# Performance work log

Measured on AMD Instinct MI355X. Metric: run time of the kernel, lower is better.

Reference implementation:

```python
import jax, jax.numpy as jnp
import numpy as np

N = 40000
IN_DIM = 128
HID = 64
E = 640000


def sage_conv(x, edge_index, W_l, b_l, W_r):
    """PyG SAGEConv with mean aggregation.
    out = lin_l(mean_{j in N(i)} x_j) + lin_r(x_i)
    edge_index[0]=src (message source), edge_index[1]=dst (aggregation target).
    """
    src, dst = edge_index[0], edge_index[1]
    n = x.shape[0]
    msgs = x[src]                                            # [E, d] gather
    sums = jax.ops.segment_sum(msgs, dst, num_segments=n)    # [N, d]
    cnt = jax.ops.segment_sum(jnp.ones((msgs.shape[0],), x.dtype), dst,
                              num_segments=n)                # [N]
    mean = sums / jnp.maximum(cnt, 1.0)[:, None]
    return mean @ W_l.T + b_l + x @ W_r.T


def setup_inputs() -> dict:
    key = jax.random.key(0)
    ks = jax.random.split(key, 8)
    x = jax.random.normal(ks[0], (N, IN_DIM), dtype=jnp.float32)
    edge_index = jax.random.randint(ks[1], (2, E), 0, N, dtype=jnp.int32)
    s1 = 1.0 / np.sqrt(IN_DIM)
    s2 = 1.0 / np.sqrt(HID)
    W1_l = jax.random.uniform(ks[2], (HID, IN_DIM), jnp.float32, -s1, s1)
    b1_l = jax.random.uniform(ks[3], (HID,), jnp.float32, -s1, s1)
    W1_r = jax.random.uniform(ks[4], (HID, IN_DIM), jnp.float32, -s1, s1)
    W2_l = jax.random.uniform(ks[5], (HID, HID), jnp.float32, -s2, s2)
    b2_l = jax.random.uniform(ks[6], (HID,), jnp.float32, -s2, s2)
    W2_r = jax.random.uniform(ks[7], (HID, HID), jnp.float32, -s2, s2)
    return {"x": x, "edge_index": edge_index,
            "W1_l": W1_l, "b1_l": b1_l, "W1_r": W1_r,
            "W2_l": W2_l, "b2_l": b2_l, "W2_r": W2_r}


def reference(x, edge_index, W1_l, b1_l, W1_r, W2_l, b2_l, W2_r):
    h = sage_conv(x, edge_index, W1_l, b1_l, W1_r)
    h = jax.nn.relu(h)
    # dropout is identity in eval mode (reference baseline is deterministic)
    z = sage_conv(h, edge_index, W2_l, b2_l, W2_r)
    return z
```

## Files before the change

kernel.cpp:

```cpp
#include <hip/hip_runtime.h>

#define INDIM 128
#define HID 64
#define CAP 64
#define GEMM_BLOCKS 625
#define BIN_BLOCKS 256
#define PREP_BLOCKS 32
#define RSH 7
#define RMASK ((1 << RSH) - 1)
#define NRANGE 313
#define SBCAP 28

__device__ __forceinline__ float bf2f(unsigned short u) {
    union { unsigned int i; float f; } c; c.i = ((unsigned int)u) << 16; return c.f;
}
__device__ __forceinline__ unsigned short f2bf(float f) {
    union { float f; unsigned int i; } c; c.f = f;
    return (unsigned short)((c.i + 0x7FFFu + ((c.i >> 16) & 1u)) >> 16);
}

__device__ __forceinline__ float4 gather4(const unsigned short* __restrict__ Pb,
                                          int row, int f4) {
    const uint2 v = *(const uint2*)&Pb[(size_t)row * 64 + f4 * 4];
    float4 r;
    r.x = bf2f((unsigned short)(v.x & 0xffffu));
    r.y = bf2f((unsigned short)(v.x >> 16));
    r.z = bf2f((unsigned short)(v.y & 0xffffu));
    r.w = bf2f((unsigned short)(v.y >> 16));
    return r;
}

__device__ __forceinline__ float4 agg_core(const unsigned short* __restrict__ Pb,
                                           int idx0, int deg, int q, int f4) {
    float4 acc = make_float4(0.f, 0.f, 0.f, 0.f);
    const int nchunk = (deg + 3) >> 2;
    for (int c = 0; c < nchunk; c += 4) {
        #pragma unroll
        for (int u = 0; u < 4; ++u) {
            const int cc = c + u;
            const int lanesel = cc * 4 + q;
            const int sidx = __shfl(idx0, lanesel, 64);
            const float m = (cc < nchunk && lanesel < deg) ? 1.f : 0.f;
            const float4 v = gather4(Pb, sidx, f4);
            acc.x += v.x * m; acc.y += v.y * m;
            acc.z += v.z * m; acc.w += v.w * m;
        }
    }
    acc.x += __shfl_xor(acc.x, 16, 64); acc.y += __shfl_xor(acc.y, 16, 64);
    acc.z += __shfl_xor(acc.z, 16, 64); acc.w += __shfl_xor(acc.w, 16, 64);
    acc.x += __shfl_xor(acc.x, 32, 64); acc.y += __shfl_xor(acc.y, 32, 64);
    acc.z += __shfl_xor(acc.z, 32, 64); acc.w += __shfl_xor(acc.w, 32, 64);
    return acc;
}


__global__ __launch_bounds__(256) void k_bin_prep(
    const int* __restrict__ src, const int* __restrict__ dst,
    unsigned int* __restrict__ hist_global, unsigned int* __restrict__ ebin,
    const float* __restrict__ W1l, const float* __restrict__ W1r,
    const float* __restrict__ W2l, const float* __restrict__ W2r,
    float* __restrict__ WT1l, float* __restrict__ WT1r,
    float* __restrict__ WT2l, float* __restrict__ WT2r, int E) {
    const int tid = threadIdx.x;

    if (blockIdx.x >= BIN_BLOCKS) {
        const int gtid = (blockIdx.x - BIN_BLOCKS) * 256 + tid;
        if (gtid < 64 * 128) {
            int j = gtid >> 7, k = gtid & 127;
            WT1l[k * 64 + j] = W1l[gtid];
            WT1r[k * 64 + j] = W1r[gtid];
        }
        if (gtid < 64 * 64) {
            int j = gtid >> 6, k = gtid & 63;
            WT2l[k * 64 + j] = W2l[gtid];
            WT2r[k * 64 + j] = W2r[gtid];
        }
        return;
    }

    __shared__ unsigned int hist[NRANGE];
    __shared__ unsigned int cur[NRANGE];
    const int b = blockIdx.x;
    const int ech = (E + BIN_BLOCKS - 1) / BIN_BLOCKS;
    const int e0 = b * ech;
    const int e1 = (e0 + ech < E) ? e0 + ech : E;

    for (int r = tid; r < NRANGE; r += 256) { hist[r] = 0; cur[r] = 0; }
    __syncthreads();
    for (int e = e0 + tid; e < e1; e += 256)
        atomicAdd(&hist[((unsigned)dst[e]) >> RSH], 1u);
    __syncthreads();
    for (int r = tid; r < NRANGE; r += 256)
        hist_global[(size_t)r * BIN_BLOCKS + b] = hist[r];
    __syncthreads();
    for (int e = e0 + tid; e < e1; e += 256) {
        const unsigned d = (unsigned)dst[e];
        const unsigned s = (unsigned)src[e];
        const unsigned r = d >> RSH;
        const unsigned off = atomicAdd(&cur[r], 1u);
        if (off < SBCAP)
            ebin[((size_t)r * BIN_BLOCKS + b) * SBCAP + off] = (d << 16) | s;
    }
}


__global__ __launch_bounds__(256) void k_gemm1_place(
    const float* __restrict__ A,
    const float* __restrict__ WTl, const float* __restrict__ WTr,
    unsigned short* __restrict__ Pb, float* __restrict__ Q,
    const unsigned int* __restrict__ hist_global,
    const unsigned int* __restrict__ ebin,
    int* __restrict__ cnt, unsigned short* __restrict__ sorted, int N) {
    __shared__ float As[64][INDIM + 1];
    __shared__ unsigned int lcnt[1 << RSH];
    const int tid = threadIdx.x;

    if (blockIdx.x >= GEMM_BLOCKS) {
        const int r = blockIdx.x - GEMM_BLOCKS;
        if (tid < (1 << RSH)) lcnt[tid] = 0;
        __syncthreads();
        unsigned c = hist_global[(size_t)r * BIN_BLOCKS + tid];
        if (c > SBCAP) c = SBCAP;
        const unsigned int* eb = ebin + ((size_t)r * BIN_BLOCKS + tid) * SBCAP;
        for (unsigned i = 0; i < c; ++i) {
            const unsigned p = eb[i];
            const unsigned d = p >> 16;
            const unsigned slot = atomicAdd(&lcnt[d & RMASK], 1u);
            if (slot < CAP)
                sorted[(d << 6) + slot] = (unsigned short)(p & 0xffffu);
        }
        __syncthreads();
        for (int l = tid; l < (1 << RSH); l += 256) {
            const int node = (r << RSH) + l;
            if (node < N) cnt[node] = (int)lcnt[l];
        }
        return;
    }

    const int bm = blockIdx.x * 64;
    for (int idx = tid; idx < 64 * 32; idx += 256) {
        int row = idx >> 5, kq = idx & 31;
        const float4 v = ((const float4*)A)[(size_t)(bm + row) * 32 + kq];
        As[row][kq * 4 + 0] = v.x; As[row][kq * 4 + 1] = v.y;
        As[row][kq * 4 + 2] = v.z; As[row][kq * 4 + 3] = v.w;
    }
    __syncthreads();

    const int tx = tid & 15, ty = tid >> 4;
    const int n0 = ty * 4;
    float accl[4][4] = {}, accr[4][4] = {};
    #pragma unroll 8
    for (int k = 0; k < INDIM; ++k) {
        float a[4];
        #pragma unroll
        for (int i = 0; i < 4; ++i) a[i] = As[n0 + i][k];
        const float4 blv = ((const float4*)WTl)[k * 16 + tx];
        const float4 brv = ((const float4*)WTr)[k * 16 + tx];
        const float bl[4] = {blv.x, blv.y, blv.z, blv.w};
        const float br[4] = {brv.x, brv.y, brv.z, brv.w};
        #pragma unroll
        for (int i = 0; i < 4; ++i) {
            #pragma unroll
            for (int j = 0; j < 4; ++j) {
                accl[i][j] += a[i] * bl[j];
                accr[i][j] += a[i] * br[j];
            }
        }
    }
    #pragma unroll
    for (int i = 0; i < 4; ++i) {
        int m = bm + n0 + i;
        ushort4 pv;
        pv.x = f2bf(accl[i][0]); pv.y = f2bf(accl[i][1]);
        pv.z = f2bf(accl[i][2]); pv.w = f2bf(accl[i][3]);
        ((ushort4*)Pb)[(size_t)m * 16 + tx] = pv;
        ((float4*)Q)[(size_t)m * 16 + tx] =
            make_float4(accr[i][0], accr[i][1], accr[i][2], accr[i][3]);
    }
}


__global__ __launch_bounds__(256) void k_agg1(
    const unsigned short* __restrict__ Pb, const float* __restrict__ Q,
    const float* __restrict__ b1,
    const int* __restrict__ cnt, const unsigned short* __restrict__ sorted,
    float* __restrict__ H, int N) {
    const int wid  = (blockIdx.x * 256 + threadIdx.x) >> 6;
    const int lane = threadIdx.x & 63;
    const int q = lane >> 4, f4 = lane & 15;
    if (wid >= N) return;
    int deg = cnt[wid]; if (deg > CAP) deg = CAP;
    const int ls = (lane < deg) ? lane : ((deg > 0) ? deg - 1 : 0);
    const int idx0 = (deg > 0) ? (int)sorted[(wid << 6) + ls] : 0;
    const float4 a = agg_core(Pb, idx0, deg, q, f4);
    if (q == 0) {
        const float inv = 1.0f / fmaxf((float)deg, 1.0f);
        const float4 qv = *(const float4*)&Q[(size_t)wid * 64 + f4 * 4];
        const float4 bv = *(const float4*)&b1[f4 * 4];
        float4 hv;
        hv.x = fmaxf(a.x * inv + bv.x + qv.x, 0.f);
        hv.y = fmaxf(a.y * inv + bv.y + qv.y, 0.f);
        hv.z = fmaxf(a.z * inv + bv.z + qv.z, 0.f);
        hv.w = fmaxf(a.w * inv + bv.w + qv.w, 0.f);
        *(float4*)&H[(size_t)wid * 64 + f4 * 4] = hv;
    }
}


__global__ __launch_bounds__(256) void k_gemm2(
    const float* __restrict__ H,
    const float* __restrict__ WTl, const float* __restrict__ WTr,
    unsigned short* __restrict__ Pb2, float* __restrict__ Q2, int N) {
    __shared__ float As[64][HID + 1];
    const int tid = threadIdx.x;
    const int bm = blockIdx.x * 64;
    for (int idx = tid; idx < 64 * 16; idx += 256) {
        int row = idx >> 4, kq = idx & 15;
        const float4 v = ((const float4*)H)[(size_t)(bm + row) * 16 + kq];
        As[row][kq * 4 + 0] = v.x; As[row][kq * 4 + 1] = v.y;
        As[row][kq * 4 + 2] = v.z; As[row][kq * 4 + 3] = v.w;
    }
    __syncthreads();

    const int tx = tid & 15, ty = tid >> 4;
    const int n0 = ty * 4;
    float accl[4][4] = {}, accr[4][4] = {};
    #pragma unroll 8
    for (int k = 0; k < HID; ++k) {
        float a[4];
        #pragma unroll
        for (int i = 0; i < 4; ++i) a[i] = As[n0 + i][k];
        const float4 blv = ((const float4*)WTl)[k * 16 + tx];
        const float4 brv = ((const float4*)WTr)[k * 16 + tx];
        const float bl[4] = {blv.x, blv.y, blv.z, blv.w};
        const float br[4] = {brv.x, brv.y, brv.z, brv.w};
        #pragma unroll
        for (int i = 0; i < 4; ++i) {
            #pragma unroll
            for (int j = 0; j < 4; ++j) {
                accl[i][j] += a[i] * bl[j];
                accr[i][j] += a[i] * br[j];
            }
        }
    }
    #pragma unroll
    for (int i = 0; i < 4; ++i) {
        int m = bm + n0 + i;
        if (m < N) {
            ushort4 pv;
            pv.x = f2bf(accl[i][0]); pv.y = f2bf(accl[i][1]);
            pv.z = f2bf(accl[i][2]); pv.w = f2bf(accl[i][3]);
            ((ushort4*)Pb2)[(size_t)m * 16 + tx] = pv;
            ((float4*)Q2)[(size_t)m * 16 + tx] =
                make_float4(accr[i][0], accr[i][1], accr[i][2], accr[i][3]);
        }
    }
}


__global__ __launch_bounds__(256) void k_agg2(
    const unsigned short* __restrict__ Pb2, const float* __restrict__ Q2,
    const float* __restrict__ b2,
    const int* __restrict__ cnt, const unsigned short* __restrict__ sorted,
    float* __restrict__ z, int N) {
    const int wid  = (blockIdx.x * 256 + threadIdx.x) >> 6;
    const int lane = threadIdx.x & 63;
    const int q = lane >> 4, f4 = lane & 15;
    if (wid >= N) return;
    int deg = cnt[wid]; if (deg > CAP) deg = CAP;
    const int ls = (lane < deg) ? lane : ((deg > 0) ? deg - 1 : 0);
    const int idx0 = (deg > 0) ? (int)sorted[(wid << 6) + ls] : 0;
    const float4 a = agg_core(Pb2, idx0, deg, q, f4);
    if (q == 0) {
        const float inv = 1.0f / fmaxf((float)deg, 1.0f);
        const float4 qv = *(const float4*)&Q2[(size_t)wid * 64 + f4 * 4];
        const float4 bv = *(const float4*)&b2[f4 * 4];
        float4 zv;
        zv.x = a.x * inv + bv.x + qv.x;
        zv.y = a.y * inv + bv.y + qv.y;
        zv.z = a.z * inv + bv.z + qv.z;
        zv.w = a.w * inv + bv.w + qv.w;
        *(float4*)&z[(size_t)wid * 64 + f4 * 4] = zv;
    }
}


extern "C" void kernel_launch(void* const* d_in, const int* in_sizes, int n_in,
                              void* d_out, int out_size, void* d_ws, size_t ws_size,
                              hipStream_t stream) {
    const float* x   = (const float*)d_in[0];
    const int*  edge = (const int*)d_in[1];
    const float* W1l = (const float*)d_in[2];
    const float* b1l = (const float*)d_in[3];
    const float* W1r = (const float*)d_in[4];
    const float* W2l = (const float*)d_in[5];
    const float* b2l = (const float*)d_in[6];
    const float* W2r = (const float*)d_in[7];

    const int N = in_sizes[0] / INDIM;
    const int E = in_sizes[1] / 2;
    const int* src = edge;
    const int* dst = edge + E;

    char* w = (char*)d_ws;
    auto carve = [&](size_t bytes) {
        char* p = w; w += (bytes + 255) & ~(size_t)255; return p;
    };
    unsigned short* Pb  = (unsigned short*)carve((size_t)N * 64 * 2);
    float* Q    = (float*)carve((size_t)N * 64 * 4);
    float* WT1l = (float*)carve(128 * 64 * 4);
    float* WT1r = (float*)carve(128 * 64 * 4);
    float* WT2l = (float*)carve(64 * 64 * 4);
    float* WT2r = (float*)carve(64 * 64 * 4);
    int* cnt    = (int*)carve((size_t)N * 4);
    unsigned short* sorted = (unsigned short*)carve((size_t)N * CAP * 2);
    unsigned int* hist_global = (unsigned int*)carve((size_t)NRANGE * BIN_BLOCKS * 4);
    size_t ebin_bytes = (size_t)NRANGE * BIN_BLOCKS * SBCAP * 4;
    size_t H_bytes    = (size_t)N * 64 * 4;
    char* uni = carve(ebin_bytes > H_bytes ? ebin_bytes : H_bytes);
    unsigned int* ebin = (unsigned int*)uni;
    float* H           = (float*)uni;

    float* zout = (float*)d_out;

    const int gT = (N + 63) / 64;
    const int gW = (N * 64 + 255) / 256;

    k_bin_prep<<<BIN_BLOCKS + PREP_BLOCKS, 256, 0, stream>>>(
        src, dst, hist_global, ebin,
        W1l, W1r, W2l, W2r, WT1l, WT1r, WT2l, WT2r, E);
    k_gemm1_place<<<GEMM_BLOCKS + NRANGE, 256, 0, stream>>>(
        x, WT1l, WT1r, Pb, Q, hist_global, ebin, cnt, sorted, N);
    k_agg1<<<gW, 256, 0, stream>>>(Pb, Q, b1l, cnt, sorted, H, N);
    k_gemm2<<<gT, 256, 0, stream>>>(H, WT2l, WT2r, Pb, Q, N);
    k_agg2<<<gW, 256, 0, stream>>>(Pb, Q, b2l, cnt, sorted, zout, N);
}
```

Before: 118.5 us.

## Fuse layer-1 aggregation with layer-2 GEMM and widen gather to 16-byte loads

The layer-1 mean aggregation and the layer-2 GEMM now run in one 512-thread kernel: each block aggregates 64 nodes into shared memory and multiplies them directly, so the H intermediate never goes to global memory. Separate Pb2/Q2 buffers are added so the fused kernel can read Pb/Q while writing the layer-2 outputs without a race. The gather now loads 8 bf16 values (16 bytes) per lane, with 8 neighbours per step instead of 4. Block order in gemm1_place is swapped so the placement blocks are scheduled first. The costs are more workspace, fewer blocks in the fused kernel, and a serial loop over 8 nodes per wave that may cut latency hiding.

```diff
diff --git a/kernel.cpp b/kernel.cpp
--- a/kernel.cpp
+++ b/kernel.cpp
@@ -19,38 +19,34 @@
     return (unsigned short)((c.i + 0x7FFFu + ((c.i >> 16) & 1u)) >> 16);
 }
 
-__device__ __forceinline__ float4 gather4(const unsigned short* __restrict__ Pb,
-                                          int row, int f4) {
-    const uint2 v = *(const uint2*)&Pb[(size_t)row * 64 + f4 * 4];
-    float4 r;
-    r.x = bf2f((unsigned short)(v.x & 0xffffu));
-    r.y = bf2f((unsigned short)(v.x >> 16));
-    r.z = bf2f((unsigned short)(v.y & 0xffffu));
-    r.w = bf2f((unsigned short)(v.y >> 16));
-    return r;
-}
-
-__device__ __forceinline__ float4 agg_core(const unsigned short* __restrict__ Pb,
-                                           int idx0, int deg, int q, int f4) {
-    float4 acc = make_float4(0.f, 0.f, 0.f, 0.f);
-    const int nchunk = (deg + 3) >> 2;
-    for (int c = 0; c < nchunk; c += 4) {
-        #pragma unroll
-        for (int u = 0; u < 4; ++u) {
-            const int cc = c + u;
-            const int lanesel = cc * 4 + q;
+__device__ __forceinline__ void agg8(const unsigned short* __restrict__ Pb,
+                                     int idx0, int deg, int q, int f8,
+                                     float acc[8]) {
+    const int nstep = (deg + 7) >> 3;
+    for (int s = 0; s < nstep; s += 2) {
+        #pragma unroll
+        for (int u = 0; u < 2; ++u) {
+            const int ss = s + u;
+            const int lanesel = ss * 8 + q;
             const int sidx = __shfl(idx0, lanesel, 64);
-            const float m = (cc < nchunk && lanesel < deg) ? 1.f : 0.f;
-            const float4 v = gather4(Pb, sidx, f4);
-            acc.x += v.x * m; acc.y += v.y * m;
-            acc.z += v.z * m; acc.w += v.w * m;
-        }
-    }
-    acc.x += __shfl_xor(acc.x, 16, 64); acc.y += __shfl_xor(acc.y, 16, 64);
-    acc.z += __shfl_xor(acc.z, 16, 64); acc.w += __shfl_xor(acc.w, 16, 64);
-    acc.x += __shfl_xor(acc.x, 32, 64); acc.y += __shfl_xor(acc.y, 32, 64);
-    acc.z += __shfl_xor(acc.z, 32, 64); acc.w += __shfl_xor(acc.w, 32, 64);
-    return acc;
+            const float m = (ss < nstep && lanesel < deg) ? 1.f : 0.f;
+            const uint4 v = *(const uint4*)&Pb[(size_t)sidx * 64 + f8 * 8];
+            acc[0] += bf2f((unsigned short)(v.x & 0xffffu)) * m;
+            acc[1] += bf2f((unsigned short)(v.x >> 16)) * m;
+            acc[2] += bf2f((unsigned short)(v.y & 0xffffu)) * m;
+            acc[3] += bf2f((unsigned short)(v.y >> 16)) * m;
+            acc[4] += bf2f((unsigned short)(v.z & 0xffffu)) * m;
+            acc[5] += bf2f((unsigned short)(v.z >> 16)) * m;
+            acc[6] += bf2f((unsigned short)(v.w & 0xffffu)) * m;
+            acc[7] += bf2f((unsigned short)(v.w >> 16)) * m;
+        }
+    }
+    #pragma unroll
+    for (int j = 0; j < 8; ++j) {
+        acc[j] += __shfl_xor(acc[j], 8, 64);
+        acc[j] += __shfl_xor(acc[j], 16, 64);
+        acc[j] += __shfl_xor(acc[j], 32, 64);
+    }
 }
 
 
@@ -115,8 +111,8 @@
     __shared__ unsigned int lcnt[1 << RSH];
     const int tid = threadIdx.x;
 
-    if (blockIdx.x >= GEMM_BLOCKS) {
-        const int r = blockIdx.x - GEMM_BLOCKS;
+    if (blockIdx.x < NRANGE) {
+        const int r = blockIdx.x;
         if (tid < (1 << RSH)) lcnt[tid] = 0;
         __syncthreads();
         unsigned c = hist_global[(size_t)r * BIN_BLOCKS + tid];
@@ -137,7 +133,7 @@
         return;
     }
 
-    const int bm = blockIdx.x * 64;
+    const int bm = (blockIdx.x - NRANGE) * 64;
     for (int idx = tid; idx < 64 * 32; idx += 256) {
         int row = idx >> 5, kq = idx & 31;
         const float4 v = ((const float4*)A)[(size_t)(bm + row) * 32 + kq];
@@ -180,62 +176,71 @@
 }
 
 
-__global__ __launch_bounds__(256) void k_agg1(
+__global__ __launch_bounds__(512) void k_agg1_gemm2(
     const unsigned short* __restrict__ Pb, const float* __restrict__ Q,
     const float* __restrict__ b1,
     const int* __restrict__ cnt, const unsigned short* __restrict__ sorted,
-    float* __restrict__ H, int N) {
-    const int wid  = (blockIdx.x * 256 + threadIdx.x) >> 6;
-    const int lane = threadIdx.x & 63;
-    const int q = lane >> 4, f4 = lane & 15;
-    if (wid >= N) return;
-    int deg = cnt[wid]; if (deg > CAP) deg = CAP;
-    const int ls = (lane < deg) ? lane : ((deg > 0) ? deg - 1 : 0);
-    const int idx0 = (deg > 0) ? (int)sorted[(wid << 6) + ls] : 0;
-    const float4 a = agg_core(Pb, idx0, deg, q, f4);
-    if (q == 0) {
-        const float inv = 1.0f / fmaxf((float)deg, 1.0f);
-        const float4 qv = *(const float4*)&Q[(size_t)wid * 64 + f4 * 4];
-        const float4 bv = *(const float4*)&b1[f4 * 4];
-        float4 hv;
-        hv.x = fmaxf(a.x * inv + bv.x + qv.x, 0.f);
-        hv.y = fmaxf(a.y * inv + bv.y + qv.y, 0.f);
-        hv.z = fmaxf(a.z * inv + bv.z + qv.z, 0.f);
-        hv.w = fmaxf(a.w * inv + bv.w + qv.w, 0.f);
-        *(float4*)&H[(size_t)wid * 64 + f4 * 4] = hv;
-    }
-}
-
-
-__global__ __launch_bounds__(256) void k_gemm2(
-    const float* __restrict__ H,
     const float* __restrict__ WTl, const float* __restrict__ WTr,
     unsigned short* __restrict__ Pb2, float* __restrict__ Q2, int N) {
-    __shared__ float As[64][HID + 1];
+    __shared__ float Hs[64][HID + 4];
     const int tid = threadIdx.x;
     const int bm = blockIdx.x * 64;
-    for (int idx = tid; idx < 64 * 16; idx += 256) {
-        int row = idx >> 4, kq = idx & 15;
-        const float4 v = ((const float4*)H)[(size_t)(bm + row) * 16 + kq];
-        As[row][kq * 4 + 0] = v.x; As[row][kq * 4 + 1] = v.y;
-        As[row][kq * 4 + 2] = v.z; As[row][kq * 4 + 3] = v.w;
+    const int lane = tid & 63, w = tid >> 6;
+    const int q = lane >> 3, f8 = lane & 7;
+    const int node_base = bm + w * 8;
+
+    int degv = (lane < 8 && node_base + lane < N) ? cnt[node_base + lane] : 0;
+    int degs[8], idx0s[8];
+    #pragma unroll
+    for (int r = 0; r < 8; ++r) {
+        int d = __shfl(degv, r, 64);
+        d = (d > CAP) ? CAP : d;
+        degs[r] = d;
+        const int ls = (lane < d) ? lane : ((d > 0) ? d - 1 : 0);
+        idx0s[r] = (d > 0) ? (int)sorted[((node_base + r) << 6) + ls] : 0;
+    }
+
+    #pragma unroll
+    for (int r = 0; r < 8; ++r) {
+        const int node = node_base + r;
+        if (node >= N) break;
+        float acc[8] = {};
+        agg8(Pb, idx0s[r], degs[r], q, f8, acc);
+        if (q == 0) {
+            const float inv = 1.0f / fmaxf((float)degs[r], 1.0f);
+            const float4 qa = *(const float4*)&Q[(size_t)node * 64 + f8 * 8];
+            const float4 qb = *(const float4*)&Q[(size_t)node * 64 + f8 * 8 + 4];
+            const float4 ba = *(const float4*)&b1[f8 * 8];
+            const float4 bb = *(const float4*)&b1[f8 * 8 + 4];
+            float4 h0, h1;
+            h0.x = fmaxf(acc[0] * inv + ba.x + qa.x, 0.f);
+            h0.y = fmaxf(acc[1] * inv + ba.y + qa.y, 0.f);
+            h0.z = fmaxf(acc[2] * inv + ba.z + qa.z, 0.f);
+            h0.w = fmaxf(acc[3] * inv + ba.w + qa.w, 0.f);
+            h1.x = fmaxf(acc[4] * inv + bb.x + qb.x, 0.f);
+            h1.y = fmaxf(acc[5] * inv + bb.y + qb.y, 0.f);
+            h1.z = fmaxf(acc[6] * inv + bb.z + qb.z, 0.f);
+            h1.w = fmaxf(acc[7] * inv + bb.w + qb.w, 0.f);
+            *(float4*)&Hs[w * 8 + r][f8 * 8] = h0;
+            *(float4*)&Hs[w * 8 + r][f8 * 8 + 4] = h1;
+        }
     }
     __syncthreads();
 
     const int tx = tid & 15, ty = tid >> 4;
-    const int n0 = ty * 4;
-    float accl[4][4] = {}, accr[4][4] = {};
+    const int n0 = ty * 2;
+    float accl[2][4] = {}, accr[2][4] = {};
     #pragma unroll 8
     for (int k = 0; k < HID; ++k) {
-        float a[4];
-        #pragma unroll
-        for (int i = 0; i < 4; ++i) a[i] = As[n0 + i][k];
+        float a[2];
+        #pragma unroll
+        for (int i = 0; i < 2; ++i) a[i] = Hs[n0 + i][k];
         const float4 blv = ((const float4*)WTl)[k * 16 + tx];
         const float4 brv = ((const float4*)WTr)[k * 16 + tx];
         const float bl[4] = {blv.x, blv.y, blv.z, blv.w};
         const float br[4] = {brv.x, brv.y, brv.z, brv.w};
         #pragma unroll
-        for (int i = 0; i < 4; ++i) {
+        for (int i = 0; i < 2; ++i) {
             #pragma unroll
             for (int j = 0; j < 4; ++j) {
                 accl[i][j] += a[i] * bl[j];
@@ -244,7 +249,7 @@
         }
     }
     #pragma unroll
-    for (int i = 0; i < 4; ++i) {
+    for (int i = 0; i < 2; ++i) {
         int m = bm + n0 + i;
         if (m < N) {
             ushort4 pv;
@@ -265,22 +270,30 @@
     float* __restrict__ z, int N) {
     const int wid  = (blockIdx.x * 256 + threadIdx.x) >> 6;
     const int lane = threadIdx.x & 63;
-    const int q = lane >> 4, f4 = lane & 15;
+    const int q = lane >> 3, f8 = lane & 7;
     if (wid >= N) return;
     int deg = cnt[wid]; if (deg > CAP) deg = CAP;
     const int ls = (lane < deg) ? lane : ((deg > 0) ? deg - 1 : 0);
     const int idx0 = (deg > 0) ? (int)sorted[(wid << 6) + ls] : 0;
-    const float4 a = agg_core(Pb2, idx0, deg, q, f4);
+    float acc[8] = {};
+    agg8(Pb2, idx0, deg, q, f8, acc);
     if (q == 0) {
         const float inv = 1.0f / fmaxf((float)deg, 1.0f);
-        const float4 qv = *(const float4*)&Q2[(size_t)wid * 64 + f4 * 4];
-        const float4 bv = *(const float4*)&b2[f4 * 4];
-        float4 zv;
-        zv.x = a.x * inv + bv.x + qv.x;
-        zv.y = a.y * inv + bv.y + qv.y;
-        zv.z = a.z * inv + bv.z + qv.z;
-        zv.w = a.w * inv + bv.w + qv.w;
-        *(float4*)&z[(size_t)wid * 64 + f4 * 4] = zv;
+        const float4 qa = *(const float4*)&Q2[(size_t)wid * 64 + f8 * 8];
+        const float4 qb = *(const float4*)&Q2[(size_t)wid * 64 + f8 * 8 + 4];
+        const float4 ba = *(const float4*)&b2[f8 * 8];
+        const float4 bb = *(const float4*)&b2[f8 * 8 + 4];
+        float4 z0, z1;
+        z0.x = acc[0] * inv + ba.x + qa.x;
+        z0.y = acc[1] * inv + ba.y + qa.y;
+        z0.z = acc[2] * inv + ba.z + qa.z;
+        z0.w = acc[3] * inv + ba.w + qa.w;
+        z1.x = acc[4] * inv + bb.x + qb.x;
+        z1.y = acc[5] * inv + bb.y + qb.y;
+        z1.z = acc[6] * inv + bb.z + qb.z;
+        z1.w = acc[7] * inv + bb.w + qb.w;
+        *(float4*)&z[(size_t)wid * 64 + f8 * 8] = z0;
+        *(float4*)&z[(size_t)wid * 64 + f8 * 8 + 4] = z1;
     }
 }
 
@@ -307,7 +320,9 @@
         char* p = w; w += (bytes + 255) & ~(size_t)255; return p;
     };
     unsigned short* Pb  = (unsigned short*)carve((size_t)N * 64 * 2);
+    unsigned short* Pb2 = (unsigned short*)carve((size_t)N * 64 * 2);
     float* Q    = (float*)carve((size_t)N * 64 * 4);
+    float* Q2   = (float*)carve((size_t)N * 64 * 4);
     float* WT1l = (float*)carve(128 * 64 * 4);
     float* WT1r = (float*)carve(128 * 64 * 4);
     float* WT2l = (float*)carve(64 * 64 * 4);
@@ -315,11 +330,7 @@
     int* cnt    = (int*)carve((size_t)N * 4);
     unsigned short* sorted = (unsigned short*)carve((size_t)N * CAP * 2);
     unsigned int* hist_global = (unsigned int*)carve((size_t)NRANGE * BIN_BLOCKS * 4);
-    size_t ebin_bytes = (size_t)NRANGE * BIN_BLOCKS * SBCAP * 4;
-    size_t H_bytes    = (size_t)N * 64 * 4;
-    char* uni = carve(ebin_bytes > H_bytes ? ebin_bytes : H_bytes);
-    unsigned int* ebin = (unsigned int*)uni;
-    float* H           = (float*)uni;
+    unsigned int* ebin = (unsigned int*)carve((size_t)NRANGE * BIN_BLOCKS * SBCAP * 4);
 
     float* zout = (float*)d_out;
 
@@ -329,9 +340,9 @@
     k_bin_prep<<<BIN_BLOCKS + PREP_BLOCKS, 256, 0, stream>>>(
         src, dst, hist_global, ebin,
         W1l, W1r, W2l, W2r, WT1l, WT1r, WT2l, WT2r, E);
-    k_gemm1_place<<<GEMM_BLOCKS + NRANGE, 256, 0, stream>>>(
+    k_gemm1_place<<<NRANGE + GEMM_BLOCKS, 256, 0, stream>>>(
         x, WT1l, WT1r, Pb, Q, hist_global, ebin, cnt, sorted, N);
-    k_agg1<<<gW, 256, 0, stream>>>(Pb, Q, b1l, cnt, sorted, H, N);
-    k_gemm2<<<gT, 256, 0, stream>>>(H, WT2l, WT2r, Pb, Q, N);
-    k_agg2<<<gW, 256, 0, stream>>>(Pb, Q, b2l, cnt, sorted, zout, N);
-}
+    k_agg1_gemm2<<<gT, 512, 0, stream>>>(Pb, Q, b1l, cnt, sorted,
+                                         WT2l, WT2r, Pb2, Q2, N);
+    k_agg2<<<gW, 256, 0, stream>>>(Pb2, Q2, b2l, cnt, sorted, zout, N);
+}
```

Result: faster. 108.3 us (-8.6%).
